# Performance work log

Hardware: AMD Instinct MI355X
Metric: run time of the kernel (lower is better)

## Reference

```python
import jax, jax.numpy as jnp
import numpy as np

N_NODES = 100000
N_EDGES = 1600000
D = 128

def setup_inputs() -> dict:
    key = jax.random.key(0)
    ks = jax.random.split(key, 8)
    s = 1.0 / np.sqrt(D)
    x = jax.random.normal(ks[0], (N_NODES, D), dtype=jnp.float32)
    edge_index = jax.random.randint(ks[1], (2, N_EDGES), 0, N_NODES, dtype=jnp.int64)
    Wl1 = jax.random.normal(ks[2], (D, D), dtype=jnp.float32) * s
    Wr1 = jax.random.normal(ks[3], (D, D), dtype=jnp.float32) * s
    b1 = jax.random.normal(ks[4], (D,), dtype=jnp.float32) * s
    Wl2 = jax.random.normal(ks[5], (D, D), dtype=jnp.float32) * s
    Wr2 = jax.random.normal(ks[6], (D, D), dtype=jnp.float32) * s
    b2 = jax.random.normal(ks[7], (D,), dtype=jnp.float32) * s
    return {"x": x, "edge_index": edge_index, "Wl1": Wl1, "Wr1": Wr1, "b1": b1,
            "Wl2": Wl2, "Wr2": Wr2, "b2": b2}

def _sage_mean(x, src, dst, n, Wl, Wr, b):
    # mean-aggregate neighbor features onto destination nodes
    msg = x[src]                                      # [E, D] gather
    agg = jax.ops.segment_sum(msg, dst, num_segments=n)  # [N, D] scatter-add
    deg = jax.ops.segment_sum(jnp.ones((src.shape[0],), x.dtype), dst, num_segments=n)
    mean = agg / jnp.maximum(deg, 1.0)[:, None]
    # SAGEConv: lin_l(aggregated) + lin_r(self), bias on lin_l
    return mean @ Wl.T + x @ Wr.T + b

def reference(x, edge_index, Wl1, Wr1, b1, Wl2, Wr2, b2):
    src, dst = edge_index[0], edge_index[1]
    n = x.shape[0]
    h = _sage_mean(x, src, dst, n, Wl1, Wr1, b1)
    h = jax.nn.relu(h)
    return _sage_mean(h, src, dst, n, Wl2, Wr2, b2)
```

## Files before the change

### kernel.cpp

```cpp
#include <hip/hip_runtime.h>
#include <hip/hip_bf16.h>

#define NN 100000
#define NE 1600000
#define DD 128

#define ASHIFT 8
#define NSPAN  256
#define BK     391
#define BCAP   4608
#define EPB    8192
#define NAB    196
#define TFH    1563
#define HELEM  800000
#define PWB    16
#define CGRID  1024

typedef __attribute__((ext_vector_type(8))) short bf16x8;
typedef __attribute__((ext_vector_type(4))) float f32x4;
typedef __attribute__((ext_vector_type(2))) float f32x2;

__device__ inline unsigned short f2bf(float f) {
    unsigned u = __builtin_bit_cast(unsigned, f);
    u += 0x7fff + ((u >> 16) & 1);
    return (unsigned short)(u >> 16);
}
__device__ inline float bf2f(unsigned short h) {
    return __builtin_bit_cast(float, (unsigned)h << 16);
}

__device__ inline void gload16(const void* g, void* l) {
    __builtin_amdgcn_global_load_lds(
        (const __attribute__((address_space(1))) unsigned int*)g,
        (__attribute__((address_space(3))) unsigned int*)l, 16, 0, 0);
}

__device__ inline void tofeat_body(int half, int blk, int t,
                                   const float* __restrict__ in,
                                   unsigned short* __restrict__ outb,
                                   unsigned char* __restrict__ out8) {
    const size_t local = (size_t)blk * 512 + t;
    if (local >= HELEM) return;
    const size_t i = (size_t)half * HELEM + local;
    const float4 a = *(const float4*)&in[i * 8];
    const float4 b = *(const float4*)&in[i * 8 + 4];
    unsigned short o[8] = {f2bf(a.x), f2bf(a.y), f2bf(a.z), f2bf(a.w),
                           f2bf(b.x), f2bf(b.y), f2bf(b.z), f2bf(b.w)};
    *(bf16x8*)&outb[i * 8] = *(bf16x8*)o;
    unsigned e0 = 0, e1 = 0;
    e0 = __builtin_amdgcn_cvt_pk_fp8_f32(a.x, a.y, e0, false);
    e0 = __builtin_amdgcn_cvt_pk_fp8_f32(a.z, a.w, e0, true);
    e1 = __builtin_amdgcn_cvt_pk_fp8_f32(b.x, b.y, e1, false);
    e1 = __builtin_amdgcn_cvt_pk_fp8_f32(b.z, b.w, e1, true);
    uint2 p = {e0, e1};
    *(uint2*)&out8[i * 8] = p;
}

__global__ __launch_bounds__(512) void fusedA2(const int* __restrict__ src,
                                               const int* __restrict__ dst,
                                               int* __restrict__ gcur,
                                               int* __restrict__ pairs,
                                               const float* __restrict__ in,
                                               unsigned short* __restrict__ outb,
                                               unsigned char* __restrict__ out8,
                                               const float* __restrict__ Wl1,
                                               const float* __restrict__ Wr1,
                                               const float* __restrict__ Wl2,
                                               const float* __restrict__ Wr2,
                                               unsigned short* __restrict__ wsb) {
    __shared__ int hist[BK];
    __shared__ int gbase[BK];
    __shared__ int lcur[BK];
    const int t = threadIdx.x;

    if (blockIdx.x >= NAB + TFH) {
        const int tid = (blockIdx.x - NAB - TFH) * 512 + t;
        const int mat = tid >> 11;
        const int ko  = (tid >> 7) & 15;
        const int j   = tid & 127;
        const float* W = (mat == 0) ? Wl1 : (mat == 1) ? Wr1 : (mat == 2) ? Wl2 : Wr2;
        const float4 w0 = *(const float4*)&W[(size_t)j * DD + ko * 8];
        const float4 w1 = *(const float4*)&W[(size_t)j * DD + ko * 8 + 4];
        unsigned short o[8] = {f2bf(w0.x), f2bf(w0.y), f2bf(w0.z), f2bf(w0.w),
                               f2bf(w1.x), f2bf(w1.y), f2bf(w1.z), f2bf(w1.w)};
        *(bf16x8*)&wsb[(size_t)tid * 8] = *(bf16x8*)o;
        return;
    }
    if (blockIdx.x >= NAB) {
        tofeat_body(0, blockIdx.x - NAB, t, in, outb, out8);
        return;
    }

    const int e0 = blockIdx.x * EPB;
    int dcache[16];
    #pragma unroll
    for (int k = 0; k < 16; ++k) {
        const int e = e0 + t + k * 512;
        dcache[k] = (e < NE) ? dst[e] : -1;
    }

    for (int i = t; i < BK; i += 512) hist[i] = 0;
    __syncthreads();
    #pragma unroll
    for (int k = 0; k < 16; ++k)
        if (dcache[k] >= 0) atomicAdd(&hist[dcache[k] >> ASHIFT], 1);
    __syncthreads();
    for (int i = t; i < BK; i += 512) {
        int c = hist[i];
        gbase[i] = i * BCAP + (c ? atomicAdd(&gcur[i], c) : 0);
        lcur[i] = 0;
    }
    __syncthreads();
    #pragma unroll
    for (int k = 0; k < 16; ++k) {
        const int e = e0 + t + k * 512;
        const int d = dcache[k];
        if (d >= 0) {
            const int b = d >> ASHIFT;
            const int r = atomicAdd(&lcur[b], 1);
            pairs[gbase[b] + r] = ((d & (NSPAN - 1)) << 17) | src[e];
        }
    }
}

__global__ __launch_bounds__(512) void fusedB2(const int* __restrict__ pairs,
                                               const int* __restrict__ gcur,
                                               int* __restrict__ cnt,
                                               int* __restrict__ rowoff,
                                               int* __restrict__ csr,
                                               const float* __restrict__ in,
                                               unsigned short* __restrict__ outb,
                                               unsigned char* __restrict__ out8) {
    __shared__ int bs[512];
    __shared__ int hist[NSPAN];
    __shared__ int scanbuf[NSPAN];
    const int t = threadIdx.x;

    if (blockIdx.x >= BK) {
        tofeat_body(1, blockIdx.x - BK, t, in, outb, out8);
        return;
    }

    const int b = blockIdx.x;
    int v = (t < BK) ? gcur[t] : 0;
    bs[t] = v;
    __syncthreads();
    #pragma unroll
    for (int d = 1; d < 512; d <<= 1) {
        int u = (t >= d) ? bs[t - d] : 0;
        __syncthreads();
        bs[t] += u;
        __syncthreads();
    }
    const int sz   = gcur[b];
    const int base = bs[b] - sz;

    const int n0    = b << ASHIFT;
    const int nodeN = min(NSPAN, NN - n0);
    const int* ep   = &pairs[(size_t)b * BCAP];

    for (int i = t; i < NSPAN; i += 512) hist[i] = 0;
    __syncthreads();
    for (int i = t; i < sz; i += 512) atomicAdd(&hist[((unsigned)ep[i]) >> 17], 1);
    __syncthreads();
    for (int i = t; i < nodeN; i += 512) cnt[n0 + i] = hist[i];
    for (int i = t; i < NSPAN; i += 512) scanbuf[i] = hist[i];
    __syncthreads();
    #pragma unroll
    for (int d = 1; d < NSPAN; d <<= 1) {
        int v0 = (t >= d && t < NSPAN) ? scanbuf[t - d] : 0;
        __syncthreads();
        if (t < NSPAN) scanbuf[t] += v0;
        __syncthreads();
    }
    for (int i = t; i < NSPAN; i += 512) {
        int excl = scanbuf[i] - hist[i];
        if (i < nodeN) rowoff[n0 + i] = base + excl;
        hist[i] = excl;
    }
    if (b == BK - 1 && t == 0) rowoff[NN] = NE;
    __syncthreads();
    for (int i = t; i < sz; i += 512) {
        int p = ep[i];
        int r = atomicAdd(&hist[((unsigned)p) >> 17], 1);
        csr[base + r] = p & 0x1FFFF;
    }
}

__device__ inline void accum8(float* a, uint2 u) {
    f32x2 p;
    p = __builtin_amdgcn_cvt_pk_f32_fp8(u.x, false); a[0] += p.x; a[1] += p.y;
    p = __builtin_amdgcn_cvt_pk_f32_fp8(u.x, true);  a[2] += p.x; a[3] += p.y;
    p = __builtin_amdgcn_cvt_pk_f32_fp8(u.y, false); a[4] += p.x; a[5] += p.y;
    p = __builtin_amdgcn_cvt_pk_f32_fp8(u.y, true);  a[6] += p.x; a[7] += p.y;
}

__global__ __launch_bounds__(256) void gather_fp8(const unsigned char* __restrict__ feat,
                                                  const int* __restrict__ rowoff,
                                                  const int* __restrict__ csr,
                                                  const int* __restrict__ cnt,
                                                  unsigned short* __restrict__ mean) {
    const int node = blockIdx.x * 16 + (threadIdx.x >> 4);
    const int l8 = (threadIdx.x & 15) * 8;
    const int beg = rowoff[node], end = rowoff[node + 1];
    float a0[8] = {0, 0, 0, 0, 0, 0, 0, 0};
    float a1[8] = {0, 0, 0, 0, 0, 0, 0, 0};
    int j = beg;
    for (; j + 7 < end; j += 8) {
        int s0 = csr[j],     s1 = csr[j + 1], s2 = csr[j + 2], s3 = csr[j + 3];
        int s4 = csr[j + 4], s5 = csr[j + 5], s6 = csr[j + 6], s7 = csr[j + 7];
        uint2 u0 = *(const uint2*)&feat[(size_t)s0 * DD + l8];
        uint2 u1 = *(const uint2*)&feat[(size_t)s1 * DD + l8];
        uint2 u2 = *(const uint2*)&feat[(size_t)s2 * DD + l8];
        uint2 u3 = *(const uint2*)&feat[(size_t)s3 * DD + l8];
        uint2 u4 = *(const uint2*)&feat[(size_t)s4 * DD + l8];
        uint2 u5 = *(const uint2*)&feat[(size_t)s5 * DD + l8];
        uint2 u6 = *(const uint2*)&feat[(size_t)s6 * DD + l8];
        uint2 u7 = *(const uint2*)&feat[(size_t)s7 * DD + l8];
        accum8(a0, u0); accum8(a1, u1); accum8(a0, u2); accum8(a1, u3);
        accum8(a0, u4); accum8(a1, u5); accum8(a0, u6); accum8(a1, u7);
    }
    for (; j + 3 < end; j += 4) {
        int s0 = csr[j], s1 = csr[j + 1], s2 = csr[j + 2], s3 = csr[j + 3];
        uint2 u0 = *(const uint2*)&feat[(size_t)s0 * DD + l8];
        uint2 u1 = *(const uint2*)&feat[(size_t)s1 * DD + l8];
        uint2 u2 = *(const uint2*)&feat[(size_t)s2 * DD + l8];
        uint2 u3 = *(const uint2*)&feat[(size_t)s3 * DD + l8];
        accum8(a0, u0); accum8(a1, u1); accum8(a0, u2); accum8(a1, u3);
    }
    for (; j < end; ++j) {
        int s0 = csr[j];
        uint2 u0 = *(const uint2*)&feat[(size_t)s0 * DD + l8];
        accum8(a0, u0);
    }
    const float inv = 1.0f / fmaxf((float)cnt[node], 1.0f);
    unsigned short o[8];
    #pragma unroll
    for (int i = 0; i < 8; ++i) o[i] = f2bf((a0[i] + a1[i]) * inv);
    *(bf16x8*)&mean[(size_t)node * DD + l8] = *(bf16x8*)o;
}

__global__ __launch_bounds__(512, 3) void combine_lds(
    const unsigned short* __restrict__ meanp, const unsigned short* __restrict__ selfp,
    const unsigned short* __restrict__ wsb,
    const float* __restrict__ bias, void* __restrict__ outp,
    unsigned char* __restrict__ out8,
    int out_bf16, int do_relu)
{
    __shared__ unsigned short sAB[2][2][2048];
    const int t = threadIdx.x;
    const int wv = t >> 6, lane = t & 63;
    const int m = lane & 15;
    const int q = lane >> 4;
    const int j0 = wv;

    const int sreg = wv >> 2;
    const int skq  = wv & 3;
    const int soff = m * 256 + skq * 64 + q * 16;

    bf16x8 bfr[2][4];
    #pragma unroll
    for (int h = 0; h < 2; ++h)
        #pragma unroll
        for (int kq = 0; kq < 4; ++kq)
            bfr[h][kq] = *(const bf16x8*)
                &wsb[((size_t)((h * 16 + kq * 4 + q) * 128) + j0 * 16 + m) * 8];

    const float bv = bias[j0 * 16 + m];

    const int NT = NN / 16;

#define STAGE(BUF, TL)                                                        \
    {                                                                         \
        const char* base_ = sreg ? (const char*)selfp : (const char*)meanp;   \
        gload16(base_ + (size_t)(TL) * 4096 + soff,                           \
                (char*)&sAB[BUF][sreg][0] + skq * 1024);                      \
    }

    int tile = blockIdx.x;
    STAGE(0, tile)
    __syncthreads();
    int cur = 0;

    for (; tile < NT; tile += CGRID) {
        const int nxt = tile + CGRID;
        if (nxt < NT) STAGE(cur ^ 1, nxt)

        f32x4 acc = (f32x4){0.f, 0.f, 0.f, 0.f};
        #pragma unroll
        for (int kq = 0; kq < 4; ++kq) {
            const bf16x8 am = *(const bf16x8*)&sAB[cur][0][kq * 512 + lane * 8];
            const bf16x8 as = *(const bf16x8*)&sAB[cur][1][kq * 512 + lane * 8];
            acc = __builtin_amdgcn_mfma_f32_16x16x32_bf16(am, bfr[0][kq], acc, 0, 0, 0);
            acc = __builtin_amdgcn_mfma_f32_16x16x32_bf16(as, bfr[1][kq], acc, 0, 0, 0);
        }

        const int col = j0 * 16 + m;
        #pragma unroll
        for (int r = 0; r < 4; ++r) {
            const size_t row = (size_t)tile * 16 + q * 4 + r;
            float v = acc[r] + bv;
            if (do_relu) v = fmaxf(v, 0.0f);
            if (out_bf16)
                ((unsigned short*)outp)[row * DD + col] = f2bf(v);
            else
                ((float*)outp)[row * DD + col] = v;
            if (out8) {
                unsigned p = __builtin_amdgcn_cvt_pk_fp8_f32(v, v, 0u, false);
                out8[row * DD + col] = (unsigned char)p;
            }
        }

        __syncthreads();
        cur ^= 1;
    }
#undef STAGE
}

extern "C" void kernel_launch(void* const* d_in, const int* in_sizes, int n_in,
                              void* d_out, int out_size, void* d_ws, size_t ws_size,
                              hipStream_t stream) {
    const float* x   = (const float*)d_in[0];
    const int*   ei  = (const int*)d_in[1];
    const float* Wl1 = (const float*)d_in[2];
    const float* Wr1 = (const float*)d_in[3];
    const float* b1  = (const float*)d_in[4];
    const float* Wl2 = (const float*)d_in[5];
    const float* Wr2 = (const float*)d_in[6];
    const float* b2  = (const float*)d_in[7];
    const int* src = ei;
    const int* dst = ei + NE;
    float* out = (float*)d_out;

    unsigned short* xb   = (unsigned short*)d_ws;
    unsigned short* mean = xb + (size_t)NN * DD;
    unsigned short* h    = mean + (size_t)NN * DD;
    unsigned char*  x8   = (unsigned char*)(h + (size_t)NN * DD);
    unsigned char*  h8   = x8 + (size_t)NN * DD;
    int*  pairs  = (int*)(h8 + (size_t)NN * DD);
    int*  gcur   = pairs + (size_t)BK * BCAP;
    int*  cnt    = gcur + BK;
    int*  rowoff = cnt + NN;
    int*  csr    = rowoff + NN + 1;
    uintptr_t wp = ((uintptr_t)(csr + NE) + 255) & ~(uintptr_t)255;
    unsigned short* wsb = (unsigned short*)wp;

    hipMemsetAsync(gcur, 0, BK * sizeof(int), stream);
    fusedA2<<<NAB + TFH + PWB, 512, 0, stream>>>(src, dst, gcur, pairs,
                                                 x, xb, x8,
                                                 Wl1, Wr1, Wl2, Wr2, wsb);
    fusedB2<<<BK + TFH, 512, 0, stream>>>(pairs, gcur, cnt, rowoff, csr, x, xb, x8);

    gather_fp8<<<NN / 16, 256, 0, stream>>>(x8, rowoff, csr, cnt, mean);
    combine_lds<<<CGRID, 512, 0, stream>>>(mean, xb, wsb, b1, h, h8, 1, 1);

    gather_fp8<<<NN / 16, 256, 0, stream>>>(h8, rowoff, csr, cnt, mean);
    combine_lds<<<CGRID, 512, 0, stream>>>(mean, h, wsb + 32768, b2, out, nullptr, 0, 0);
}
```

Before: 254.1 us.

## Store fp8 features as 32-column panels and map gather panels to XCD pairs

The fp8 feature copies (x8 and h8) now use a panel-major layout: four panels of 32 columns, each of size NN×32. The gather kernel is restructured so each block handles one panel for 64 nodes. Block indices are mapped so each XCD pair works on a single panel, with each XCD in the pair taking half the nodes. The goal is to shrink the working set each XCD's L2 sees during random neighbor gathers and so raise cache hit rates. In exchange, each gathered row is only 8 bytes per thread across 4 lanes, and there are four times as many index reads per node.

```diff
diff --git a/kernel.cpp b/kernel.cpp
--- a/kernel.cpp
+++ b/kernel.cpp
@@ -15,6 +15,7 @@
 #define HELEM  800000
 #define PWB    16
 #define CGRID  1024
+#define GPB    782
 
 typedef __attribute__((ext_vector_type(8))) short bf16x8;
 typedef __attribute__((ext_vector_type(4))) float f32x4;
@@ -53,7 +54,11 @@
     e1 = __builtin_amdgcn_cvt_pk_fp8_f32(b.x, b.y, e1, false);
     e1 = __builtin_amdgcn_cvt_pk_fp8_f32(b.z, b.w, e1, true);
     uint2 p = {e0, e1};
-    *(uint2*)&out8[i * 8] = p;
+    const size_t n = i >> 4;
+    const int    c = (int)(i & 15);
+    const int    pn = c >> 2;
+    const int    off = (c & 3) * 8;
+    *(uint2*)&out8[((size_t)pn * NN + n) * 32 + off] = p;
 }
 
 __global__ __launch_bounds__(512) void fusedA2(const int* __restrict__ src,
@@ -195,13 +200,23 @@
     p = __builtin_amdgcn_cvt_pk_f32_fp8(u.y, true);  a[6] += p.x; a[7] += p.y;
 }
 
-__global__ __launch_bounds__(256) void gather_fp8(const unsigned char* __restrict__ feat,
-                                                  const int* __restrict__ rowoff,
-                                                  const int* __restrict__ csr,
-                                                  const int* __restrict__ cnt,
-                                                  unsigned short* __restrict__ mean) {
-    const int node = blockIdx.x * 16 + (threadIdx.x >> 4);
-    const int l8 = (threadIdx.x & 15) * 8;
+__global__ __launch_bounds__(256) void gather_panel(const unsigned char* __restrict__ feat,
+                                                    const int* __restrict__ rowoff,
+                                                    const int* __restrict__ csr,
+                                                    const int* __restrict__ cnt,
+                                                    unsigned short* __restrict__ mean) {
+    const int b      = blockIdx.x;
+    const int xcd    = b & 7;
+    const int panel  = xcd >> 1;
+    const int parity = xcd & 1;
+    const int local  = b >> 3;
+    const int t = threadIdx.x;
+    const int node = parity * 50000 + local * 64 + (t >> 2);
+    const int limit = parity ? NN : 50000;
+    if (node >= limit) return;
+    const int l8 = (t & 3) * 8;
+    const unsigned char* fp = feat + (size_t)panel * NN * 32;
+
     const int beg = rowoff[node], end = rowoff[node + 1];
     float a0[8] = {0, 0, 0, 0, 0, 0, 0, 0};
     float a1[8] = {0, 0, 0, 0, 0, 0, 0, 0};
@@ -209,35 +224,35 @@
     for (; j + 7 < end; j += 8) {
         int s0 = csr[j],     s1 = csr[j + 1], s2 = csr[j + 2], s3 = csr[j + 3];
         int s4 = csr[j + 4], s5 = csr[j + 5], s6 = csr[j + 6], s7 = csr[j + 7];
-        uint2 u0 = *(const uint2*)&feat[(size_t)s0 * DD + l8];
-        uint2 u1 = *(const uint2*)&feat[(size_t)s1 * DD + l8];
-        uint2 u2 = *(const uint2*)&feat[(size_t)s2 * DD + l8];
-        uint2 u3 = *(const uint2*)&feat[(size_t)s3 * DD + l8];
-        uint2 u4 = *(const uint2*)&feat[(size_t)s4 * DD + l8];
-        uint2 u5 = *(const uint2*)&feat[(size_t)s5 * DD + l8];
-        uint2 u6 = *(const uint2*)&feat[(size_t)s6 * DD + l8];
-        uint2 u7 = *(const uint2*)&feat[(size_t)s7 * DD + l8];
+        uint2 u0 = *(const uint2*)&fp[(size_t)s0 * 32 + l8];
+        uint2 u1 = *(const uint2*)&fp[(size_t)s1 * 32 + l8];
+        uint2 u2 = *(const uint2*)&fp[(size_t)s2 * 32 + l8];
+        uint2 u3 = *(const uint2*)&fp[(size_t)s3 * 32 + l8];
+        uint2 u4 = *(const uint2*)&fp[(size_t)s4 * 32 + l8];
+        uint2 u5 = *(const uint2*)&fp[(size_t)s5 * 32 + l8];
+        uint2 u6 = *(const uint2*)&fp[(size_t)s6 * 32 + l8];
+        uint2 u7 = *(const uint2*)&fp[(size_t)s7 * 32 + l8];
         accum8(a0, u0); accum8(a1, u1); accum8(a0, u2); accum8(a1, u3);
         accum8(a0, u4); accum8(a1, u5); accum8(a0, u6); accum8(a1, u7);
     }
     for (; j + 3 < end; j += 4) {
         int s0 = csr[j], s1 = csr[j + 1], s2 = csr[j + 2], s3 = csr[j + 3];
-        uint2 u0 = *(const uint2*)&feat[(size_t)s0 * DD + l8];
-        uint2 u1 = *(const uint2*)&feat[(size_t)s1 * DD + l8];
-        uint2 u2 = *(const uint2*)&feat[(size_t)s2 * DD + l8];
-        uint2 u3 = *(const uint2*)&feat[(size_t)s3 * DD + l8];
+        uint2 u0 = *(const uint2*)&fp[(size_t)s0 * 32 + l8];
+        uint2 u1 = *(const uint2*)&fp[(size_t)s1 * 32 + l8];
+        uint2 u2 = *(const uint2*)&fp[(size_t)s2 * 32 + l8];
+        uint2 u3 = *(const uint2*)&fp[(size_t)s3 * 32 + l8];
         accum8(a0, u0); accum8(a1, u1); accum8(a0, u2); accum8(a1, u3);
     }
     for (; j < end; ++j) {
         int s0 = csr[j];
-        uint2 u0 = *(const uint2*)&feat[(size_t)s0 * DD + l8];
+        uint2 u0 = *(const uint2*)&fp[(size_t)s0 * 32 + l8];
         accum8(a0, u0);
     }
     const float inv = 1.0f / fmaxf((float)cnt[node], 1.0f);
     unsigned short o[8];
     #pragma unroll
     for (int i = 0; i < 8; ++i) o[i] = f2bf((a0[i] + a1[i]) * inv);
-    *(bf16x8*)&mean[(size_t)node * DD + l8] = *(bf16x8*)o;
+    *(bf16x8*)&mean[(size_t)node * DD + panel * 32 + (t & 3) * 8] = *(bf16x8*)o;
 }
 
 __global__ __launch_bounds__(512, 3) void combine_lds(
@@ -269,6 +284,8 @@
     const float bv = bias[j0 * 16 + m];
 
     const int NT = NN / 16;
+    const int opan = wv >> 1;
+    const int ooff = (wv & 1) * 16 + m;
 
 #define STAGE(BUF, TL)                                                        \
     {                                                                         \
@@ -307,7 +324,7 @@
                 ((float*)outp)[row * DD + col] = v;
             if (out8) {
                 unsigned p = __builtin_amdgcn_cvt_pk_fp8_f32(v, v, 0u, false);
-                out8[row * DD + col] = (unsigned char)p;
+                out8[((size_t)opan * NN + row) * 32 + ooff] = (unsigned char)p;
             }
         }
 
@@ -351,9 +368,9 @@
                                                  Wl1, Wr1, Wl2, Wr2, wsb);
     fusedB2<<<BK + TFH, 512, 0, stream>>>(pairs, gcur, cnt, rowoff, csr, x, xb, x8);
 
-    gather_fp8<<<NN / 16, 256, 0, stream>>>(x8, rowoff, csr, cnt, mean);
+    gather_panel<<<8 * GPB, 256, 0, stream>>>(x8, rowoff, csr, cnt, mean);
     combine_lds<<<CGRID, 512, 0, stream>>>(mean, xb, wsb, b1, h, h8, 1, 1);
 
-    gather_fp8<<<NN / 16, 256, 0, stream>>>(h8, rowoff, csr, cnt, mean);
+    gather_panel<<<8 * GPB, 256, 0, stream>>>(h8, rowoff, csr, cnt, mean);
     combine_lds<<<CGRID, 512, 0, stream>>>(mean, h, wsb + 32768, b2, out, nullptr, 0, 0);
 }
```

Result: slower. 280.2 us (+10.2%).
